# Optimization experiments

Measured on AMD Instinct MI355X. Metric: run time of the kernel, lower is better.

Reference implementation:

```python
import jax, jax.numpy as jnp
import numpy as np

DIM = 1024
HEADS = 16
DIM_HEAD = 64
INNER = HEADS * DIM_HEAD  # 1024
FF_INNER = 4 * DIM        # 4096
EPS = 1e-5


def _ln(t, gamma):
    mu = jnp.mean(t, axis=-1, keepdims=True)
    var = jnp.var(t, axis=-1, keepdims=True)
    return (t - mu) * jax.lax.rsqrt(var + EPS) * gamma


def setup_inputs() -> dict:
    key = jax.random.key(0)
    ks = jax.random.split(key, 8)
    B, N = 4, 1024
    s = 0.02
    return {
        "x": jax.random.normal(ks[0], (B, N, DIM), dtype=jnp.float32),
        "y": jax.random.normal(ks[1], (B, N, DIM), dtype=jnp.float32),
        "g1": jnp.ones((DIM,), dtype=jnp.float32),
        "g2": jnp.ones((DIM,), dtype=jnp.float32),
        "g_out": jnp.ones((DIM,), dtype=jnp.float32),
        "Wq": jax.random.normal(ks[2], (DIM, INNER), dtype=jnp.float32) * s,
        "Wkv": jax.random.normal(ks[3], (DIM, 2 * DIM_HEAD), dtype=jnp.float32) * s,
        "Wo": jax.random.normal(ks[4], (INNER, DIM), dtype=jnp.float32) * s,
        "Wff1": jax.random.normal(ks[5], (DIM, 2 * FF_INNER), dtype=jnp.float32) * s,
        "Wff2": jax.random.normal(ks[6], (FF_INNER, DIM), dtype=jnp.float32) * s,
    }


def reference(x, y, g1, g2, g_out, Wq, Wkv, Wo, Wff1, Wff2):
    B, N, _ = x.shape
    scale = DIM_HEAD ** -0.5
    xn = _ln(x, g1)
    yn = _ln(y, g2)  # note: torch code rebinds y = norm2(y); residual & FF use normed y
    # multi-query attention: per-head queries, single shared k/v head
    q = (xn @ Wq).reshape(B, N, HEADS, DIM_HEAD).transpose(0, 2, 1, 3) * scale  # b h n d
    kv = yn @ Wkv  # b j (2d)
    k, v = kv[..., :DIM_HEAD], kv[..., DIM_HEAD:]
    sim = jnp.einsum('bhid,bjd->bhij', q, k)
    attn = jax.nn.softmax(sim, axis=-1)  # torch code subtracts amax then softmax; identical math
    out = jnp.einsum('bhij,bjd->bhid', attn, v)
    out = out.transpose(0, 2, 1, 3).reshape(B, N, INNER)
    out = out @ Wo
    out = _ln(out + yn, g_out)
    # SwiGLU FFN on normed y: first half is value, second half is gate
    h = yn @ Wff1
    val, gate = h[..., :FF_INNER], h[..., FF_INNER:]
    ff = (jax.nn.silu(gate) * val) @ Wff2
    return out + ff
```

## Files before the change

kernel.cpp:

```cpp
#include <hip/hip_runtime.h>
#include <hip/hip_bf16.h>


typedef __attribute__((ext_vector_type(8))) short bf16x8;
typedef __attribute__((ext_vector_type(4))) short s16x4;
typedef __attribute__((ext_vector_type(4))) float f32x4;

__device__ __forceinline__ short f2b(float f) {
  union { float f; unsigned u; } v; v.f = f;
  unsigned r = (v.u + 0x7fffu + ((v.u >> 16) & 1u)) >> 16;
  return (short)r;
}

__device__ __forceinline__ void gload16(const short* g, short* l) {
  __builtin_amdgcn_global_load_lds(
      (const __attribute__((address_space(1))) void*)g,
      (__attribute__((address_space(3))) void*)l, 16, 0, 0);
}

__global__ __launch_bounds__(256) void cvtT_kernel(const float* __restrict__ in,
                                                   short* __restrict__ out,
                                                   int K, int N) {
  __shared__ float tile[32][33];
  int n0 = blockIdx.x * 32, k0 = blockIdx.y * 32;
  int tx = threadIdx.x & 7, ty = threadIdx.x >> 3;
  float4 v = *(const float4*)&in[(size_t)(k0 + ty) * N + n0 + tx * 4];
  tile[ty][tx * 4 + 0] = v.x;
  tile[ty][tx * 4 + 1] = v.y;
  tile[ty][tx * 4 + 2] = v.z;
  tile[ty][tx * 4 + 3] = v.w;
  __syncthreads();
  s16x4 o = { f2b(tile[tx * 4 + 0][ty]), f2b(tile[tx * 4 + 1][ty]),
              f2b(tile[tx * 4 + 2][ty]), f2b(tile[tx * 4 + 3][ty]) };
  *(s16x4*)&out[(size_t)(n0 + ty) * K + k0 + tx * 4] = o;
}

__global__ __launch_bounds__(256) void ln_kernel(const float* __restrict__ in,
                                                 const float* __restrict__ gamma,
                                                 short* __restrict__ out16,
                                                 float* __restrict__ out32) {
  int row = blockIdx.x;
  int t = threadIdx.x;
  float4 v = ((const float4*)(in + (size_t)row * 1024))[t];
  float s  = v.x + v.y + v.z + v.w;
  float sq = v.x*v.x + v.y*v.y + v.z*v.z + v.w*v.w;
  __shared__ float ssum[256], ssq[256];
  ssum[t] = s; ssq[t] = sq;
  __syncthreads();
  for (int o = 128; o > 0; o >>= 1) {
    if (t < o) { ssum[t] += ssum[t + o]; ssq[t] += ssq[t + o]; }
    __syncthreads();
  }
  float mu  = ssum[0] * (1.0f / 1024.0f);
  float var = ssq[0] * (1.0f / 1024.0f) - mu * mu;
  float rs  = rsqrtf(var + 1e-5f);
  float4 g = ((const float4*)gamma)[t];
  float o0 = (v.x - mu) * rs * g.x;
  float o1 = (v.y - mu) * rs * g.y;
  float o2 = (v.z - mu) * rs * g.z;
  float o3 = (v.w - mu) * rs * g.w;
  if (out16) {
    s16x4 o = { f2b(o0), f2b(o1), f2b(o2), f2b(o3) };
    ((s16x4*)out16)[(size_t)row * 256 + t] = o;
  }
  if (out32) {
    float4 o = { o0, o1, o2, o3 };
    ((float4*)out32)[(size_t)row * 256 + t] = o;
  }
}

template<int EPI, int BM, int BN>
__global__ __launch_bounds__(256, 2) void gemm_ring(
    const short* __restrict__ A, const short* __restrict__ B,
    int M, int N, int Kstride, int Klen,
    short* __restrict__ out16, float* __restrict__ out32,
    const float* __restrict__ res, float scale)
{
  constexpr int DEPTH = 4;
  constexpr int FM = BM / 32;
  constexpr int FN = BN / 32;
  constexpr int AL = BM / 64;
  constexpr int BL = BN / 64;
  __shared__ __align__(16) short As[DEPTH][BM * 32];
  __shared__ __align__(16) short Bs[DEPTH][BN * 32];

  int t = threadIdx.x;
  int lane = t & 63, wave = t >> 6;
  int wm = wave >> 1, wn = wave & 1;
  int lrow = lane & 15, lgrp = lane >> 4;
  int m0 = blockIdx.y * BM, n0 = blockIdx.x * BN;
  int kbase = blockIdx.z * Klen;

  int srow = lane >> 2, scol = (lane & 3) * 8;
  const short* gA = A + (size_t)(m0 + wave * 16 + srow) * Kstride + kbase + scol;
  const short* gB = B + (size_t)(n0 + wave * 16 + srow) * Kstride + kbase + scol;

  auto STAGE = [&](int slot, int kt) {
    int k0 = kt * 32;
#pragma unroll
    for (int i = 0; i < AL; i++)
      gload16(gA + (size_t)(i * 64) * Kstride + k0, &As[slot][(i * 4 + wave) * 512]);
#pragma unroll
    for (int j = 0; j < BL; j++)
      gload16(gB + (size_t)(j * 64) * Kstride + k0, &Bs[slot][(j * 4 + wave) * 512]);
  };

  f32x4 acc[FM][FN];
  const f32x4 zero = { 0.f, 0.f, 0.f, 0.f };
#pragma unroll
  for (int i = 0; i < FM; i++)
#pragma unroll
    for (int j = 0; j < FN; j++) acc[i][j] = zero;

  int nt = Klen / 32;
#pragma unroll
  for (int p = 0; p < DEPTH - 1; p++) STAGE(p, p);

  int slot = 0, stage_slot = DEPTH - 1;
  for (int tI = 0; tI < nt; ++tI) {
    int rem = nt - 1 - tI;
    if constexpr (AL + BL == 4) {
      if (rem >= 2)      asm volatile("s_waitcnt vmcnt(8)" ::: "memory");
      else if (rem == 1) asm volatile("s_waitcnt vmcnt(4)" ::: "memory");
      else               asm volatile("s_waitcnt vmcnt(0)" ::: "memory");
    } else {
      if (rem >= 2)      asm volatile("s_waitcnt vmcnt(6)" ::: "memory");
      else if (rem == 1) asm volatile("s_waitcnt vmcnt(3)" ::: "memory");
      else               asm volatile("s_waitcnt vmcnt(0)" ::: "memory");
    }
    __builtin_amdgcn_s_barrier();
    __builtin_amdgcn_sched_barrier(0);

    if (tI + DEPTH - 1 < nt) STAGE(stage_slot, tI + DEPTH - 1);

    bf16x8 af[FM], bfr[FN];
#pragma unroll
    for (int mf = 0; mf < FM; mf++)
      af[mf] = *(const bf16x8*)&As[slot][(wm * (BM / 2) + mf * 16 + lrow) * 32 + lgrp * 8];
#pragma unroll
    for (int nf = 0; nf < FN; nf++)
      bfr[nf] = *(const bf16x8*)&Bs[slot][(wn * (BN / 2) + nf * 16 + lrow) * 32 + lgrp * 8];

    __builtin_amdgcn_s_setprio(1);
#pragma unroll
    for (int mf = 0; mf < FM; mf++)
#pragma unroll
      for (int nf = 0; nf < FN; nf++)
        acc[mf][nf] = __builtin_amdgcn_mfma_f32_16x16x32_bf16(af[mf], bfr[nf], acc[mf][nf], 0, 0, 0);
    __builtin_amdgcn_s_setprio(0);

    slot = (slot + 1 == DEPTH) ? 0 : slot + 1;
    stage_slot = (stage_slot + 1 == DEPTH) ? 0 : stage_slot + 1;
  }

#pragma unroll
  for (int mf = 0; mf < FM; mf++)
#pragma unroll
    for (int nf = 0; nf < FN; nf++)
#pragma unroll
      for (int r = 0; r < 4; r++) {
        int row = m0 + wm * (BM / 2) + mf * 16 + lgrp * 4 + r;
        int col = n0 + wn * (BN / 2) + nf * 16 + lrow;
        float v = acc[mf][nf][r];
        if (EPI == 0) {
          out16[(size_t)row * N + col] = f2b(v * scale);
        } else if (EPI == 1) {
          out32[(size_t)row * N + col] = v + res[(size_t)row * N + col];
        } else {
          out32[(size_t)blockIdx.z * M * N + (size_t)row * N + col] = v;
        }
      }
}

__global__ __launch_bounds__(512, 2) void gemm_ff1(
    const short* __restrict__ A, const short* __restrict__ B,
    short* __restrict__ out16)
{
  constexpr int K = 1024, NT = 32;
  __shared__ __align__(16) short As[4][256 * 32];
  __shared__ __align__(16) short Bv[4][128 * 32];
  __shared__ __align__(16) short Bg[4][128 * 32];

  int t = threadIdx.x;
  int lane = t & 63, wave = t >> 6;
  int wm = wave >> 1, wn = wave & 1;
  int lrow = lane & 15, lgrp = lane >> 4;
  int m0 = blockIdx.y * 256, n0 = blockIdx.x * 128;

  int srow = lane >> 2, scol = (lane & 3) * 8;
  const short* gA  = A + (size_t)(m0 + wave * 16 + srow) * K + scol;
  const short* gBv = B + (size_t)(n0 + wave * 16 + srow) * K + scol;
  const short* gBg = B + (size_t)(4096 + n0 + wave * 16 + srow) * K + scol;

  f32x4 acc[4][4], acc2[4][4];
  const f32x4 zero = { 0.f, 0.f, 0.f, 0.f };
#pragma unroll
  for (int i = 0; i < 4; i++)
#pragma unroll
    for (int j = 0; j < 4; j++) { acc[i][j] = zero; acc2[i][j] = zero; }

#pragma unroll
  for (int p = 0; p < 3; p++) {
    gload16(gA + p * 32,                      &As[p][wave * 512]);
    gload16(gA + (size_t)128 * K + p * 32,    &As[p][4096 + wave * 512]);
    gload16(gBv + p * 32,                     &Bv[p][wave * 512]);
    gload16(gBg + p * 32,                     &Bg[p][wave * 512]);
  }

  for (int tI = 0; tI < NT; ++tI) {
    int slot = tI & 3, s3 = (tI + 3) & 3;
    bool pf = (tI + 3 < NT);
    int k3 = (tI + 3) * 32;
    int rem = NT - 1 - tI;
    if (rem >= 2)      asm volatile("s_waitcnt vmcnt(8)" ::: "memory");
    else if (rem == 1) asm volatile("s_waitcnt vmcnt(4)" ::: "memory");
    else               asm volatile("s_waitcnt vmcnt(0)" ::: "memory");
    __builtin_amdgcn_s_barrier();
    __builtin_amdgcn_sched_barrier(0);

    bf16x8 af[4], bv[4], bg[4];
#pragma unroll
    for (int mf = 0; mf < 4; mf++)
      af[mf] = *(const bf16x8*)&As[slot][(wm * 64 + mf * 16 + lrow) * 32 + lgrp * 8];
    bv[0] = *(const bf16x8*)&Bv[slot][(wn * 64 + lrow) * 32 + lgrp * 8];
    bv[1] = *(const bf16x8*)&Bv[slot][(wn * 64 + 16 + lrow) * 32 + lgrp * 8];
    if (pf) gload16(gA + k3, &As[s3][wave * 512]);
    __builtin_amdgcn_s_barrier();
    __builtin_amdgcn_sched_barrier(0);
    __builtin_amdgcn_s_setprio(1);
#pragma unroll
    for (int mf = 0; mf < 4; mf++) {
      acc[mf][0] = __builtin_amdgcn_mfma_f32_16x16x32_bf16(af[mf], bv[0], acc[mf][0], 0, 0, 0);
      acc[mf][1] = __builtin_amdgcn_mfma_f32_16x16x32_bf16(af[mf], bv[1], acc[mf][1], 0, 0, 0);
    }
    __builtin_amdgcn_s_setprio(0);
    __builtin_amdgcn_s_barrier();
    __builtin_amdgcn_sched_barrier(0);
    bv[2] = *(const bf16x8*)&Bv[slot][(wn * 64 + 32 + lrow) * 32 + lgrp * 8];
    bv[3] = *(const bf16x8*)&Bv[slot][(wn * 64 + 48 + lrow) * 32 + lgrp * 8];
    if (pf) gload16(gA + (size_t)128 * K + k3, &As[s3][4096 + wave * 512]);
    __builtin_amdgcn_s_barrier();
    __builtin_amdgcn_sched_barrier(0);
    __builtin_amdgcn_s_setprio(1);
#pragma unroll
    for (int mf = 0; mf < 4; mf++) {
      acc[mf][2] = __builtin_amdgcn_mfma_f32_16x16x32_bf16(af[mf], bv[2], acc[mf][2], 0, 0, 0);
      acc[mf][3] = __builtin_amdgcn_mfma_f32_16x16x32_bf16(af[mf], bv[3], acc[mf][3], 0, 0, 0);
    }
    __builtin_amdgcn_s_setprio(0);
    __builtin_amdgcn_s_barrier();
    __builtin_amdgcn_sched_barrier(0);
    bg[0] = *(const bf16x8*)&Bg[slot][(wn * 64 + lrow) * 32 + lgrp * 8];
    bg[1] = *(const bf16x8*)&Bg[slot][(wn * 64 + 16 + lrow) * 32 + lgrp * 8];
    if (pf) gload16(gBv + k3, &Bv[s3][wave * 512]);
    __builtin_amdgcn_s_barrier();
    __builtin_amdgcn_sched_barrier(0);
    __builtin_amdgcn_s_setprio(1);
#pragma unroll
    for (int mf = 0; mf < 4; mf++) {
      acc2[mf][0] = __builtin_amdgcn_mfma_f32_16x16x32_bf16(af[mf], bg[0], acc2[mf][0], 0, 0, 0);
      acc2[mf][1] = __builtin_amdgcn_mfma_f32_16x16x32_bf16(af[mf], bg[1], acc2[mf][1], 0, 0, 0);
    }
    __builtin_amdgcn_s_setprio(0);
    __builtin_amdgcn_s_barrier();
    __builtin_amdgcn_sched_barrier(0);
    bg[2] = *(const bf16x8*)&Bg[slot][(wn * 64 + 32 + lrow) * 32 + lgrp * 8];
    bg[3] = *(const bf16x8*)&Bg[slot][(wn * 64 + 48 + lrow) * 32 + lgrp * 8];
    if (pf) gload16(gBg + k3, &Bg[s3][wave * 512]);
    __builtin_amdgcn_s_barrier();
    __builtin_amdgcn_sched_barrier(0);
    __builtin_amdgcn_s_setprio(1);
#pragma unroll
    for (int mf = 0; mf < 4; mf++) {
      acc2[mf][2] = __builtin_amdgcn_mfma_f32_16x16x32_bf16(af[mf], bg[2], acc2[mf][2], 0, 0, 0);
      acc2[mf][3] = __builtin_amdgcn_mfma_f32_16x16x32_bf16(af[mf], bg[3], acc2[mf][3], 0, 0, 0);
    }
    __builtin_amdgcn_s_setprio(0);
    __builtin_amdgcn_s_barrier();
    __builtin_amdgcn_sched_barrier(0);
  }

#pragma unroll
  for (int mf = 0; mf < 4; mf++)
#pragma unroll
    for (int nf = 0; nf < 4; nf++)
#pragma unroll
      for (int r = 0; r < 4; r++) {
        int row = m0 + wm * 64 + mf * 16 + lgrp * 4 + r;
        int col = n0 + wn * 64 + nf * 16 + lrow;
        float v = acc[mf][nf][r];
        float gate = acc2[mf][nf][r];
        float sig = 1.0f / (1.0f + __expf(-gate));
        out16[(size_t)row * 4096 + col] = f2b(v * gate * sig);
      }
}

__global__ __launch_bounds__(256) void kvred_kernel(const float* __restrict__ p,
                                                    short* __restrict__ out, int n4) {
  int i = blockIdx.x * 256 + threadIdx.x;
  if (i >= n4) return;
  const int S = 4096 * 128 / 4;
  float4 a = ((const float4*)p)[i];
  float4 b = ((const float4*)p)[i + S];
  float4 c = ((const float4*)p)[i + 2 * S];
  float4 d = ((const float4*)p)[i + 3 * S];
  s16x4 o = { f2b(a.x + b.x + c.x + d.x), f2b(a.y + b.y + c.y + d.y),
              f2b(a.z + b.z + c.z + d.z), f2b(a.w + b.w + c.w + d.w) };
  ((s16x4*)out)[i] = o;
}

__global__ __launch_bounds__(256) void attn_kernel(const short* __restrict__ q,
                                                   const short* __restrict__ kv,
                                                   short* __restrict__ ao)
{
  __shared__ __align__(16) short Ks[64 * 64];
  __shared__ __align__(16) short Vs[64 * 64];
  __shared__ __align__(16) short Ps[4][32 * 64];

  int t = threadIdx.x;
  int lane = t & 63, wave = t >> 6;
  int lrow = lane & 15, lgrp = lane >> 4;
  int qt = blockIdx.x;
  int b = blockIdx.y >> 2, hg = blockIdx.y & 3;
  int h = hg * 4 + wave;

  char* Kb = (char*)Ks;
  char* Vb = (char*)Vs;
  char* Pb = (char*)Ps + wave * (32 * 64 * 2);

  bf16x8 qf[2][2];
  const short* qb = q + ((size_t)(b * 1024 + qt * 32)) * 1024 + h * 64;
#pragma unroll
  for (int mf = 0; mf < 2; mf++)
#pragma unroll
    for (int kk = 0; kk < 2; kk++)
      qf[mf][kk] = *(const bf16x8*)&qb[(size_t)(mf * 16 + lrow) * 1024 + kk * 32 + lgrp * 8];

  f32x4 oacc[2][4];
  float m_[2][4], l_[2][4];
  const f32x4 zero = { 0.f, 0.f, 0.f, 0.f };
#pragma unroll
  for (int i = 0; i < 2; i++)
#pragma unroll
    for (int j = 0; j < 4; j++) { oacc[i][j] = zero; }
#pragma unroll
  for (int i = 0; i < 2; i++)
#pragma unroll
    for (int r = 0; r < 4; r++) { m_[i][r] = -3.0e38f; l_[i][r] = 0.f; }

  int4 d[4];
  {
    const short* kvb = kv + ((size_t)(b * 1024 + lane)) * 128 + wave * 32;
#pragma unroll
    for (int i = 0; i < 4; i++) d[i] = ((const int4*)kvb)[i];
  }

  for (int j0 = 0; j0 < 1024; j0 += 64) {
    __syncthreads();
    if (wave < 2) {
      int sw = (lane & 7) << 4;
#pragma unroll
      for (int i = 0; i < 4; i++)
        *(int4*)(Kb + lane * 128 + ((wave * 64 + i * 16) ^ sw)) = d[i];
    } else {
#pragma unroll
      for (int i = 0; i < 4; i++) {
        union { int4 v; short s[8]; } u; u.v = d[i];
#pragma unroll
        for (int j = 0; j < 8; j++) {
          int dd = (wave - 2) * 32 + i * 8 + j;
          *(short*)(Vb + dd * 128 + ((lane * 2) ^ ((dd & 7) << 4))) = u.s[j];
        }
      }
    }
    if (j0 + 64 < 1024) {
      const short* kvn = kv + ((size_t)(b * 1024 + j0 + 64 + lane)) * 128 + wave * 32;
#pragma unroll
      for (int i = 0; i < 4; i++) d[i] = ((const int4*)kvn)[i];
    }
    __syncthreads();

    bf16x8 kf[4][2];
#pragma unroll
    for (int nf = 0; nf < 4; nf++) {
      int row = nf * 16 + lrow, sw = (row & 7) << 4;
      kf[nf][0] = *(const bf16x8*)(Kb + row * 128 + ((lgrp * 16) ^ sw));
      kf[nf][1] = *(const bf16x8*)(Kb + row * 128 + ((64 + lgrp * 16) ^ sw));
    }
    f32x4 sacc[2][4];
#pragma unroll
    for (int i = 0; i < 2; i++)
#pragma unroll
      for (int j = 0; j < 4; j++) sacc[i][j] = zero;
    __builtin_amdgcn_s_setprio(1);
#pragma unroll
    for (int mf = 0; mf < 2; mf++)
#pragma unroll
      for (int nf = 0; nf < 4; nf++)
#pragma unroll
        for (int kk = 0; kk < 2; kk++)
          sacc[mf][nf] = __builtin_amdgcn_mfma_f32_16x16x32_bf16(qf[mf][kk], kf[nf][kk], sacc[mf][nf], 0, 0, 0);
    __builtin_amdgcn_s_setprio(0);

    float pmax[2][4];
    bool okd = true;
#pragma unroll
    for (int mf = 0; mf < 2; mf++)
#pragma unroll
      for (int r = 0; r < 4; r++) {
        float pm = fmaxf(fmaxf(sacc[mf][0][r], sacc[mf][1][r]),
                         fmaxf(sacc[mf][2][r], sacc[mf][3][r]));
        pmax[mf][r] = pm;
        okd = okd && (pm <= m_[mf][r] + 8.0f);
      }
    if (__all(okd)) {
#pragma unroll
      for (int mf = 0; mf < 2; mf++)
#pragma unroll
        for (int r = 0; r < 4; r++) {
          int row = mf * 16 + lgrp * 4 + r, sw = (row & 7) << 4;
          float al = 0.f;
#pragma unroll
          for (int nf = 0; nf < 4; nf++) {
            float p = __expf(sacc[mf][nf][r] - m_[mf][r]);
            *(short*)(Pb + row * 128 + (((nf * 16 + lrow) * 2) ^ sw)) = f2b(p);
            al += p;
          }
          l_[mf][r] += al;
        }
    } else {
#pragma unroll
      for (int mf = 0; mf < 2; mf++)
#pragma unroll
        for (int r = 0; r < 4; r++) {
          float mx = pmax[mf][r];
#pragma unroll
          for (int o = 8; o >= 1; o >>= 1) mx = fmaxf(mx, __shfl_xor(mx, o));
          float mnew = fmaxf(m_[mf][r], mx);
          float corr = __expf(m_[mf][r] - mnew);
          int row = mf * 16 + lgrp * 4 + r, sw = (row & 7) << 4;
          float al = 0.f;
#pragma unroll
          for (int nf = 0; nf < 4; nf++) {
            float p = __expf(sacc[mf][nf][r] - mnew);
            *(short*)(Pb + row * 128 + (((nf * 16 + lrow) * 2) ^ sw)) = f2b(p);
            al += p;
          }
          l_[mf][r] = l_[mf][r] * corr + al;
          m_[mf][r] = mnew;
#pragma unroll
          for (int nf = 0; nf < 4; nf++) oacc[mf][nf][r] *= corr;
        }
    }

    bf16x8 vf[4][2], pfr[2][2];
#pragma unroll
    for (int nf = 0; nf < 4; nf++) {
      int row = nf * 16 + lrow, sw = (row & 7) << 4;
      vf[nf][0] = *(const bf16x8*)(Vb + row * 128 + ((lgrp * 16) ^ sw));
      vf[nf][1] = *(const bf16x8*)(Vb + row * 128 + ((64 + lgrp * 16) ^ sw));
    }
#pragma unroll
    for (int mf = 0; mf < 2; mf++) {
      int row = mf * 16 + lrow, sw = (row & 7) << 4;
      pfr[mf][0] = *(const bf16x8*)(Pb + row * 128 + ((lgrp * 16) ^ sw));
      pfr[mf][1] = *(const bf16x8*)(Pb + row * 128 + ((64 + lgrp * 16) ^ sw));
    }
    __builtin_amdgcn_s_setprio(1);
#pragma unroll
    for (int mf = 0; mf < 2; mf++)
#pragma unroll
      for (int nf = 0; nf < 4; nf++)
#pragma unroll
        for (int kk = 0; kk < 2; kk++)
          oacc[mf][nf] = __builtin_amdgcn_mfma_f32_16x16x32_bf16(pfr[mf][kk], vf[nf][kk], oacc[mf][nf], 0, 0, 0);
    __builtin_amdgcn_s_setprio(0);
  }

#pragma unroll
  for (int mf = 0; mf < 2; mf++)
#pragma unroll
    for (int r = 0; r < 4; r++) {
      float ls = l_[mf][r];
#pragma unroll
      for (int o = 8; o >= 1; o >>= 1) ls += __shfl_xor(ls, o);
      float inv = 1.0f / ls;
      int qrow = qt * 32 + mf * 16 + lgrp * 4 + r;
#pragma unroll
      for (int nf = 0; nf < 4; nf++) {
        float val = oacc[mf][nf][r] * inv;
        ao[((size_t)(b * 1024 + qrow)) * 1024 + h * 64 + nf * 16 + lrow] = f2b(val);
      }
    }
}

extern "C" void kernel_launch(void* const* d_in, const int* in_sizes, int n_in,
                              void* d_out, int out_size, void* d_ws, size_t ws_size,
                              hipStream_t stream) {
  const float* x     = (const float*)d_in[0];
  const float* y     = (const float*)d_in[1];
  const float* g1    = (const float*)d_in[2];
  const float* g2    = (const float*)d_in[3];
  const float* g_out = (const float*)d_in[4];
  const float* Wq    = (const float*)d_in[5];
  const float* Wkv   = (const float*)d_in[6];
  const float* Wo    = (const float*)d_in[7];
  const float* Wff1  = (const float*)d_in[8];
  const float* Wff2  = (const float*)d_in[9];

  char* ws = (char*)d_ws;
  size_t off = 0;
  auto alloc = [&](size_t bytes) { char* p = ws + off; off += bytes; return p; };
  short* wqT    = (short*)alloc((size_t)1024 * 1024 * 2);
  short* wkvT   = (short*)alloc((size_t)128 * 1024 * 2);
  short* woT    = (short*)alloc((size_t)1024 * 1024 * 2);
  short* wff1T  = (short*)alloc((size_t)8192 * 1024 * 2);
  short* wff2T  = (short*)alloc((size_t)1024 * 4096 * 2);
  short* xn16   = (short*)alloc((size_t)4096 * 1024 * 2);
  short* yn16   = (short*)alloc((size_t)4096 * 1024 * 2);
  float* ynf    = (float*)alloc((size_t)4096 * 1024 * 4);
  short* q16    = (short*)alloc((size_t)4096 * 1024 * 2);
  short* kv16   = (short*)alloc((size_t)4096 * 128 * 2);
  short* ao16   = (short*)alloc((size_t)4096 * 1024 * 2);
  float* lnout  = (float*)alloc((size_t)4096 * 1024 * 4);
  short* act16  = (short*)alloc((size_t)4096 * 4096 * 2);
  float* kvpart = (float*)alloc((size_t)4 * 4096 * 128 * 4);
  float* outf   = (float*)d_out;

  cvtT_kernel<<<dim3(1024 / 32, 1024 / 32), 256, 0, stream>>>(Wq,   wqT,   1024, 1024);
  cvtT_kernel<<<dim3(128 / 32, 1024 / 32),  256, 0, stream>>>(Wkv,  wkvT,  1024, 128);
  cvtT_kernel<<<dim3(1024 / 32, 1024 / 32), 256, 0, stream>>>(Wo,   woT,   1024, 1024);
  cvtT_kernel<<<dim3(8192 / 32, 1024 / 32), 256, 0, stream>>>(Wff1, wff1T, 1024, 8192);
  cvtT_kernel<<<dim3(1024 / 32, 4096 / 32), 256, 0, stream>>>(Wff2, wff2T, 4096, 1024);

  ln_kernel<<<4096, 256, 0, stream>>>(x, g1, xn16, nullptr);
  ln_kernel<<<4096, 256, 0, stream>>>(y, g2, yn16, ynf);

  gemm_ring<0, 64, 128><<<dim3(8, 64), 256, 0, stream>>>(
      xn16, wqT, 4096, 1024, 1024, 1024, q16, nullptr, nullptr, 0.125f);
  gemm_ring<3, 64, 128><<<dim3(1, 64, 4), 256, 0, stream>>>(
      yn16, wkvT, 4096, 128, 1024, 256, nullptr, kvpart, nullptr, 1.0f);
  kvred_kernel<<<512, 256, 0, stream>>>(kvpart, kv16, 4096 * 128 / 4);

  attn_kernel<<<dim3(32, 16), 256, 0, stream>>>(q16, kv16, ao16);

  gemm_ring<1, 64, 128><<<dim3(8, 64), 256, 0, stream>>>(
      ao16, woT, 4096, 1024, 1024, 1024, nullptr, outf, ynf, 1.0f);

  ln_kernel<<<4096, 256, 0, stream>>>(outf, g_out, nullptr, lnout);

  gemm_ff1<<<dim3(32, 16), 512, 0, stream>>>(yn16, wff1T, act16);

  gemm_ring<1, 64, 128><<<dim3(8, 64), 256, 0, stream>>>(
      act16, wff2T, 4096, 1024, 4096, 4096, nullptr, outf, lnout, 1.0f);
}
```

Measured before the change: 324.6 us.

## Restructure FF1 SwiGLU GEMM to K=64 double-buffer with XOR-swizzled LDS and 2x4 warp grid

The fused FF1 SwiGLU GEMM moves from a 4-stage pipeline with K-step 32 to a 2-stage double buffer with K-step 64. This halves the number of main-loop iterations and barrier rounds. LDS tiles now use an XOR swizzle on 16-byte chunks to avoid bank conflicts on the wider rows. The wave layout changes from 4x2 to 2x4, so each wave owns 128x32 outputs (8x2 fragments) instead of 64x64. The cost is a shallower prefetch, with a full vmcnt(0) wait and barrier at the end of each iteration, plus more A-fragment registers per wave.

After: 316.7 us. -2.4%, faster.

```diff
diff --git a/kernel.cpp b/kernel.cpp
--- a/kernel.cpp
+++ b/kernel.cpp
@@ -176,118 +176,144 @@
     const short* __restrict__ A, const short* __restrict__ B,
     short* __restrict__ out16)
 {
-  constexpr int K = 1024, NT = 32;
-  __shared__ __align__(16) short As[4][256 * 32];
-  __shared__ __align__(16) short Bv[4][128 * 32];
-  __shared__ __align__(16) short Bg[4][128 * 32];
+  constexpr int K = 1024, NT = 16;
+  __shared__ __align__(16) short As[2][256 * 64];
+  __shared__ __align__(16) short Bv[2][128 * 64];
+  __shared__ __align__(16) short Bg[2][128 * 64];
 
   int t = threadIdx.x;
   int lane = t & 63, wave = t >> 6;
-  int wm = wave >> 1, wn = wave & 1;
+  int wm = wave >> 2, wn = wave & 3;
   int lrow = lane & 15, lgrp = lane >> 4;
   int m0 = blockIdx.y * 256, n0 = blockIdx.x * 128;
 
-  int srow = lane >> 2, scol = (lane & 3) * 8;
-  const short* gA  = A + (size_t)(m0 + wave * 16 + srow) * K + scol;
-  const short* gBv = B + (size_t)(n0 + wave * 16 + srow) * K + scol;
-  const short* gBg = B + (size_t)(4096 + n0 + wave * 16 + srow) * K + scol;
-
-  f32x4 acc[4][4], acc2[4][4];
+  int srow8 = lane >> 3;
+  int schunk = ((lane & 7) ^ srow8) * 8;
+  const short* gA  = A + (size_t)(m0 + wave * 8 + srow8) * K + schunk;
+  const short* gBv = B + (size_t)(n0 + wave * 8 + srow8) * K + schunk;
+  const short* gBg = B + (size_t)(4096 + n0 + wave * 8 + srow8) * K + schunk;
+
+  f32x4 acc[8][2], acc2[8][2];
   const f32x4 zero = { 0.f, 0.f, 0.f, 0.f };
 #pragma unroll
+  for (int i = 0; i < 8; i++) {
+    acc[i][0] = zero; acc[i][1] = zero; acc2[i][0] = zero; acc2[i][1] = zero;
+  }
+
+  int rc0 = ((lgrp) ^ (lrow & 7)) * 8;
+  int rc1 = ((4 | lgrp) ^ (lrow & 7)) * 8;
+
+#pragma unroll
   for (int i = 0; i < 4; i++)
-#pragma unroll
-    for (int j = 0; j < 4; j++) { acc[i][j] = zero; acc2[i][j] = zero; }
-
-#pragma unroll
-  for (int p = 0; p < 3; p++) {
-    gload16(gA + p * 32,                      &As[p][wave * 512]);
-    gload16(gA + (size_t)128 * K + p * 32,    &As[p][4096 + wave * 512]);
-    gload16(gBv + p * 32,                     &Bv[p][wave * 512]);
-    gload16(gBg + p * 32,                     &Bg[p][wave * 512]);
-  }
+    gload16(gA + (size_t)(i * 64) * K, &As[0][(i * 64 + wave * 8) * 64]);
+#pragma unroll
+  for (int j = 0; j < 2; j++) {
+    gload16(gBv + (size_t)(j * 64) * K, &Bv[0][(j * 64 + wave * 8) * 64]);
+    gload16(gBg + (size_t)(j * 64) * K, &Bg[0][(j * 64 + wave * 8) * 64]);
+  }
+  asm volatile("s_waitcnt vmcnt(0)" ::: "memory");
+  __builtin_amdgcn_s_barrier();
+  __builtin_amdgcn_sched_barrier(0);
 
   for (int tI = 0; tI < NT; ++tI) {
-    int slot = tI & 3, s3 = (tI + 3) & 3;
-    bool pf = (tI + 3 < NT);
-    int k3 = (tI + 3) * 32;
-    int rem = NT - 1 - tI;
-    if (rem >= 2)      asm volatile("s_waitcnt vmcnt(8)" ::: "memory");
-    else if (rem == 1) asm volatile("s_waitcnt vmcnt(4)" ::: "memory");
-    else               asm volatile("s_waitcnt vmcnt(0)" ::: "memory");
-    __builtin_amdgcn_s_barrier();
-    __builtin_amdgcn_sched_barrier(0);
-
-    bf16x8 af[4], bv[4], bg[4];
-#pragma unroll
-    for (int mf = 0; mf < 4; mf++)
-      af[mf] = *(const bf16x8*)&As[slot][(wm * 64 + mf * 16 + lrow) * 32 + lgrp * 8];
-    bv[0] = *(const bf16x8*)&Bv[slot][(wn * 64 + lrow) * 32 + lgrp * 8];
-    bv[1] = *(const bf16x8*)&Bv[slot][(wn * 64 + 16 + lrow) * 32 + lgrp * 8];
-    if (pf) gload16(gA + k3, &As[s3][wave * 512]);
-    __builtin_amdgcn_s_barrier();
-    __builtin_amdgcn_sched_barrier(0);
-    __builtin_amdgcn_s_setprio(1);
-#pragma unroll
-    for (int mf = 0; mf < 4; mf++) {
-      acc[mf][0] = __builtin_amdgcn_mfma_f32_16x16x32_bf16(af[mf], bv[0], acc[mf][0], 0, 0, 0);
-      acc[mf][1] = __builtin_amdgcn_mfma_f32_16x16x32_bf16(af[mf], bv[1], acc[mf][1], 0, 0, 0);
-    }
-    __builtin_amdgcn_s_setprio(0);
-    __builtin_amdgcn_s_barrier();
-    __builtin_amdgcn_sched_barrier(0);
-    bv[2] = *(const bf16x8*)&Bv[slot][(wn * 64 + 32 + lrow) * 32 + lgrp * 8];
-    bv[3] = *(const bf16x8*)&Bv[slot][(wn * 64 + 48 + lrow) * 32 + lgrp * 8];
-    if (pf) gload16(gA + (size_t)128 * K + k3, &As[s3][4096 + wave * 512]);
-    __builtin_amdgcn_s_barrier();
-    __builtin_amdgcn_sched_barrier(0);
-    __builtin_amdgcn_s_setprio(1);
-#pragma unroll
-    for (int mf = 0; mf < 4; mf++) {
-      acc[mf][2] = __builtin_amdgcn_mfma_f32_16x16x32_bf16(af[mf], bv[2], acc[mf][2], 0, 0, 0);
-      acc[mf][3] = __builtin_amdgcn_mfma_f32_16x16x32_bf16(af[mf], bv[3], acc[mf][3], 0, 0, 0);
-    }
-    __builtin_amdgcn_s_setprio(0);
-    __builtin_amdgcn_s_barrier();
-    __builtin_amdgcn_sched_barrier(0);
-    bg[0] = *(const bf16x8*)&Bg[slot][(wn * 64 + lrow) * 32 + lgrp * 8];
-    bg[1] = *(const bf16x8*)&Bg[slot][(wn * 64 + 16 + lrow) * 32 + lgrp * 8];
-    if (pf) gload16(gBv + k3, &Bv[s3][wave * 512]);
-    __builtin_amdgcn_s_barrier();
-    __builtin_amdgcn_sched_barrier(0);
-    __builtin_amdgcn_s_setprio(1);
-#pragma unroll
-    for (int mf = 0; mf < 4; mf++) {
-      acc2[mf][0] = __builtin_amdgcn_mfma_f32_16x16x32_bf16(af[mf], bg[0], acc2[mf][0], 0, 0, 0);
-      acc2[mf][1] = __builtin_amdgcn_mfma_f32_16x16x32_bf16(af[mf], bg[1], acc2[mf][1], 0, 0, 0);
-    }
-    __builtin_amdgcn_s_setprio(0);
-    __builtin_amdgcn_s_barrier();
-    __builtin_amdgcn_sched_barrier(0);
-    bg[2] = *(const bf16x8*)&Bg[slot][(wn * 64 + 32 + lrow) * 32 + lgrp * 8];
-    bg[3] = *(const bf16x8*)&Bg[slot][(wn * 64 + 48 + lrow) * 32 + lgrp * 8];
-    if (pf) gload16(gBg + k3, &Bg[s3][wave * 512]);
-    __builtin_amdgcn_s_barrier();
-    __builtin_amdgcn_sched_barrier(0);
-    __builtin_amdgcn_s_setprio(1);
-#pragma unroll
-    for (int mf = 0; mf < 4; mf++) {
-      acc2[mf][2] = __builtin_amdgcn_mfma_f32_16x16x32_bf16(af[mf], bg[2], acc2[mf][2], 0, 0, 0);
-      acc2[mf][3] = __builtin_amdgcn_mfma_f32_16x16x32_bf16(af[mf], bg[3], acc2[mf][3], 0, 0, 0);
-    }
-    __builtin_amdgcn_s_setprio(0);
-    __builtin_amdgcn_s_barrier();
-    __builtin_amdgcn_sched_barrier(0);
-  }
-
-#pragma unroll
-  for (int mf = 0; mf < 4; mf++)
-#pragma unroll
-    for (int nf = 0; nf < 4; nf++)
+    int cur = tI & 1, nxt = cur ^ 1;
+    bool pf = (tI + 1 < NT);
+    int kn = (tI + 1) * 64;
+    bf16x8 af0[8], af1[8], bvf[2], bgf[2];
+
+#pragma unroll
+    for (int mf = 0; mf < 8; mf++)
+      af0[mf] = *(const bf16x8*)&As[cur][(wm * 128 + mf * 16 + lrow) * 64 + rc0];
+    bvf[0] = *(const bf16x8*)&Bv[cur][(wn * 32 + lrow) * 64 + rc0];
+    bvf[1] = *(const bf16x8*)&Bv[cur][(wn * 32 + 16 + lrow) * 64 + rc0];
+    if (pf) {
+      gload16(gA + kn,                     &As[nxt][(wave * 8) * 64]);
+      gload16(gA + (size_t)64 * K + kn,    &As[nxt][(64 + wave * 8) * 64]);
+      gload16(gA + (size_t)128 * K + kn,   &As[nxt][(128 + wave * 8) * 64]);
+    }
+    __builtin_amdgcn_s_barrier();
+    asm volatile("s_waitcnt lgkmcnt(0)" ::: "memory");
+    __builtin_amdgcn_sched_barrier(0);
+    __builtin_amdgcn_s_setprio(1);
+#pragma unroll
+    for (int mf = 0; mf < 8; mf++) {
+      acc[mf][0] = __builtin_amdgcn_mfma_f32_16x16x32_bf16(af0[mf], bvf[0], acc[mf][0], 0, 0, 0);
+      acc[mf][1] = __builtin_amdgcn_mfma_f32_16x16x32_bf16(af0[mf], bvf[1], acc[mf][1], 0, 0, 0);
+    }
+    __builtin_amdgcn_s_setprio(0);
+    __builtin_amdgcn_s_barrier();
+    __builtin_amdgcn_sched_barrier(0);
+
+#pragma unroll
+    for (int mf = 0; mf < 8; mf++)
+      af1[mf] = *(const bf16x8*)&As[cur][(wm * 128 + mf * 16 + lrow) * 64 + rc1];
+    bvf[0] = *(const bf16x8*)&Bv[cur][(wn * 32 + lrow) * 64 + rc1];
+    bvf[1] = *(const bf16x8*)&Bv[cur][(wn * 32 + 16 + lrow) * 64 + rc1];
+    if (pf) {
+      gload16(gA + (size_t)192 * K + kn,   &As[nxt][(192 + wave * 8) * 64]);
+      gload16(gBv + kn,                    &Bv[nxt][(wave * 8) * 64]);
+      gload16(gBv + (size_t)64 * K + kn,   &Bv[nxt][(64 + wave * 8) * 64]);
+    }
+    __builtin_amdgcn_s_barrier();
+    asm volatile("s_waitcnt lgkmcnt(0)" ::: "memory");
+    __builtin_amdgcn_sched_barrier(0);
+    __builtin_amdgcn_s_setprio(1);
+#pragma unroll
+    for (int mf = 0; mf < 8; mf++) {
+      acc[mf][0] = __builtin_amdgcn_mfma_f32_16x16x32_bf16(af1[mf], bvf[0], acc[mf][0], 0, 0, 0);
+      acc[mf][1] = __builtin_amdgcn_mfma_f32_16x16x32_bf16(af1[mf], bvf[1], acc[mf][1], 0, 0, 0);
+    }
+    __builtin_amdgcn_s_setprio(0);
+    __builtin_amdgcn_s_barrier();
+    __builtin_amdgcn_sched_barrier(0);
+
+    bgf[0] = *(const bf16x8*)&Bg[cur][(wn * 32 + lrow) * 64 + rc0];
+    bgf[1] = *(const bf16x8*)&Bg[cur][(wn * 32 + 16 + lrow) * 64 + rc0];
+    if (pf) {
+      gload16(gBg + kn,                    &Bg[nxt][(wave * 8) * 64]);
+      gload16(gBg + (size_t)64 * K + kn,   &Bg[nxt][(64 + wave * 8) * 64]);
+    }
+    __builtin_amdgcn_s_barrier();
+    asm volatile("s_waitcnt lgkmcnt(0)" ::: "memory");
+    __builtin_amdgcn_sched_barrier(0);
+    __builtin_amdgcn_s_setprio(1);
+#pragma unroll
+    for (int mf = 0; mf < 8; mf++) {
+      acc2[mf][0] = __builtin_amdgcn_mfma_f32_16x16x32_bf16(af0[mf], bgf[0], acc2[mf][0], 0, 0, 0);
+      acc2[mf][1] = __builtin_amdgcn_mfma_f32_16x16x32_bf16(af0[mf], bgf[1], acc2[mf][1], 0, 0, 0);
+    }
+    __builtin_amdgcn_s_setprio(0);
+    __builtin_amdgcn_s_barrier();
+    __builtin_amdgcn_sched_barrier(0);
+
+    bgf[0] = *(const bf16x8*)&Bg[cur][(wn * 32 + lrow) * 64 + rc1];
+    bgf[1] = *(const bf16x8*)&Bg[cur][(wn * 32 + 16 + lrow) * 64 + rc1];
+    __builtin_amdgcn_s_barrier();
+    asm volatile("s_waitcnt lgkmcnt(0)" ::: "memory");
+    __builtin_amdgcn_sched_barrier(0);
+    __builtin_amdgcn_s_setprio(1);
+#pragma unroll
+    for (int mf = 0; mf < 8; mf++) {
+      acc2[mf][0] = __builtin_amdgcn_mfma_f32_16x16x32_bf16(af1[mf], bgf[0], acc2[mf][0], 0, 0, 0);
+      acc2[mf][1] = __builtin_amdgcn_mfma_f32_16x16x32_bf16(af1[mf], bgf[1], acc2[mf][1], 0, 0, 0);
+    }
+    __builtin_amdgcn_s_setprio(0);
+    __builtin_amdgcn_s_barrier();
+    __builtin_amdgcn_sched_barrier(0);
+
+    asm volatile("s_waitcnt vmcnt(0)" ::: "memory");
+    __builtin_amdgcn_s_barrier();
+    __builtin_amdgcn_sched_barrier(0);
+  }
+
+#pragma unroll
+  for (int mf = 0; mf < 8; mf++)
+#pragma unroll
+    for (int nf = 0; nf < 2; nf++)
 #pragma unroll
       for (int r = 0; r < 4; r++) {
-        int row = m0 + wm * 64 + mf * 16 + lgrp * 4 + r;
-        int col = n0 + wn * 64 + nf * 16 + lrow;
+        int row = m0 + wm * 128 + mf * 16 + lgrp * 4 + r;
+        int col = n0 + wn * 32 + nf * 16 + lrow;
         float v = acc[mf][nf][r];
         float gate = acc2[mf][nf][r];
         float sig = 1.0f / (1.0f + __expf(-gate));
```
